# Kernel optimization log

Hardware: AMD Instinct MI355X
Metric: run time of the kernel (lower is better)

Reference implementation:

```python
import jax, jax.numpy as jnp
import numpy as np

E = 64        # first-level branches / experts
N_LEAF = 1024 # leaves per branch (item id = branch*N_LEAF + leaf; zero trajectory = (0,0))
K = 10        # output_list_size


def setup_inputs() -> dict:
    key = jax.random.key(0)
    ks = jax.random.split(key, 8)
    s = 0.05
    B, D, H = 256, 256, 512
    return {
        "state": jax.random.normal(ks[0], (B, D), jnp.float32),
        # root policy (outputs E branch logits)
        "rW1": jax.random.normal(ks[1], (D, H), jnp.float32) * s,
        "rb1": jnp.zeros((H,), jnp.float32),
        "rW2": jax.random.normal(ks[2], (H, H), jnp.float32) * s,
        "rb2": jnp.zeros((H,), jnp.float32),
        "rW3": jax.random.normal(ks[3], (H, E), jnp.float32) * s,
        "rb3": jnp.zeros((E,), jnp.float32),
        # stacked per-branch expert policies (each outputs N_LEAF logits)
        "eW1": jax.random.normal(ks[4], (E, D, H), jnp.float32) * s,
        "eb1": jnp.zeros((E, H), jnp.float32),
        "eW2": jax.random.normal(ks[5], (E, H, H), jnp.float32) * s,
        "eb2": jnp.zeros((E, H), jnp.float32),
        "eW3": jax.random.normal(ks[6], (E, H, N_LEAF), jnp.float32) * s,
        "eb3": jnp.zeros((E, N_LEAF), jnp.float32),
    }


def reference(state, rW1, rb1, rW2, rb2, rW3, rb3, eW1, eb1, eW2, eb2, eW3, eb3):
    # deterministic=True path, mask_items=None
    B = state.shape[0]
    relu = jax.nn.relu
    # root policy: MLP -> branch logits [B, E]
    h = relu(state @ rW1 + rb1)
    h = relu(h @ rW2 + rb2)
    root_logits = h @ rW3 + rb3
    idx = jnp.argmax(root_logits, axis=-1)                       # top-1 branch per sample [B]
    root_lp = jax.nn.log_softmax(root_logits, axis=-1)[jnp.arange(B), idx]  # [B]
    # top-1 routed expert forward: gather per-sample expert weights (MoE dispatch)
    h1 = relu(jnp.einsum('bi,bih->bh', state, eW1[idx]) + eb1[idx])
    h2 = relu(jnp.einsum('bh,bhg->bg', h1, eW2[idx]) + eb2[idx])
    logits = jnp.einsum('bg,bgn->bn', h2, eW3[idx]) + eb3[idx]   # [B, N_LEAF]
    lp = jax.nn.log_softmax(logits, axis=-1)
    # top-(k+1), then drop leaf 0 if this sample routed to branch 0 (the id-0 trajectory)
    _, top_idx = jax.lax.top_k(logits, K + 1)                    # [B, K+1]
    keep = ~((top_idx == 0) & (idx[:, None] == 0))
    order = jnp.argsort(~keep, axis=1, stable=True)              # kept entries first, order preserved
    item_idx = jnp.take_along_axis(top_idx, order[:, :K], axis=1)  # [B, K]
    final_lp = jnp.take_along_axis(lp, item_idx, axis=1) + root_lp[:, None]  # [B, K]
    traj = jnp.stack([jnp.broadcast_to(idx[:, None], (B, K)), item_idx], axis=-1)  # [B, K, 2]
    return traj, final_lp
```

## Files before the change

kernel.cpp:

```cpp
#include <hip/hip_runtime.h>
#include <math.h>

#define Bn 256
#define Dm 256
#define Hm 512
#define Em 64
#define NL 1024
#define TOPK 10
#define GS 8
#define MAXG 88

template<int IN, int OUT, int MT, int XPARTS, bool GROUPED>
__global__ __launch_bounds__(512) void dense_ks4(
        const float* __restrict__ X, const int* __restrict__ perm,
        const float* __restrict__ Bin, int bin_estride,
        const float* __restrict__ W, const int4* __restrict__ groups,
        float* __restrict__ Y) {
    constexpr int NW = 8, KQ = IN / 4, KCH = KQ / NW, CCH = 256, NR = 4;

    int e, p0, cnt;
    if (GROUPED) {
        const int4 g = groups[blockIdx.x];
        if (g.z == 0) return;
        e = g.x; p0 = g.y; cnt = g.z;
    } else {
        e = 0; p0 = blockIdx.x * MT; cnt = MT;
    }
    const int kq = blockIdx.z;
    const int kbase = kq * KQ;

    __shared__ float sxT[KQ * MT];
    __shared__ float part[NR * MT * CCH];
    const int tid = threadIdx.x;

    for (int j = tid; j < (KQ / 4) * MT; j += 512) {
        const int c  = j & (MT - 1);
        const int i4 = j / MT;
        float4 x = make_float4(0.f, 0.f, 0.f, 0.f);
        if (c < cnt) {
            const int row = perm ? perm[p0 + c] : (p0 + c);
            const size_t off = (size_t)row * IN + kbase + i4 * 4;
            x = *(const float4*)(X + off);
            #pragma unroll
            for (int pb = 1; pb < XPARTS; ++pb) {
                const float4 xp = *(const float4*)(X + (size_t)pb * Bn * IN + off);
                x.x += xp.x; x.y += xp.y; x.z += xp.z; x.w += xp.w;
            }
            if (Bin) {
                const float4 b = *(const float4*)(Bin + (size_t)e * bin_estride + kbase + i4 * 4);
                x.x = fmaxf(x.x + b.x, 0.f); x.y = fmaxf(x.y + b.y, 0.f);
                x.z = fmaxf(x.z + b.z, 0.f); x.w = fmaxf(x.w + b.w, 0.f);
            }
        }
        sxT[(i4 * 4 + 0) * MT + c] = x.x;
        sxT[(i4 * 4 + 1) * MT + c] = x.y;
        sxT[(i4 * 4 + 2) * MT + c] = x.z;
        sxT[(i4 * 4 + 3) * MT + c] = x.w;
    }
    __syncthreads();

    const int wave = tid >> 6, lane = tid & 63;
    const int colb = blockIdx.y * CCH;
    const int col  = colb + lane * 4;
    const int k0   = wave * KCH;
    const float* We = W + (size_t)e * IN * OUT + (size_t)(kbase + k0) * OUT + col;

    float acc[MT][4];
    #pragma unroll
    for (int c = 0; c < MT; ++c) { acc[c][0]=0.f; acc[c][1]=0.f; acc[c][2]=0.f; acc[c][3]=0.f; }

    #pragma unroll 4
    for (int i = 0; i < KCH; ++i) {
        const float4 w = *(const float4*)(We + (size_t)i * OUT);
        const float* xr = &sxT[(k0 + i) * MT];
        const float4 xa = *(const float4*)xr;
        const float4 xb = *(const float4*)(xr + 4);
        const float xs[8] = {xa.x, xa.y, xa.z, xa.w, xb.x, xb.y, xb.z, xb.w};
        #pragma unroll
        for (int c = 0; c < 8; ++c) {
            acc[c][0] = fmaf(xs[c], w.x, acc[c][0]);
            acc[c][1] = fmaf(xs[c], w.y, acc[c][1]);
            acc[c][2] = fmaf(xs[c], w.z, acc[c][2]);
            acc[c][3] = fmaf(xs[c], w.w, acc[c][3]);
        }
    }

    if (wave < NR) {
        #pragma unroll
        for (int c = 0; c < MT; ++c)
            *(float4*)&part[((wave * MT) + c) * CCH + lane * 4] = *(const float4*)acc[c];
    }
    __syncthreads();
    if (wave >= NR) {
        #pragma unroll
        for (int c = 0; c < MT; ++c) {
            float4* pp = (float4*)&part[(((wave - NR) * MT) + c) * CCH + lane * 4];
            float4 v = *pp;
            v.x += acc[c][0]; v.y += acc[c][1]; v.z += acc[c][2]; v.w += acc[c][3];
            *pp = v;
        }
    }
    __syncthreads();

    float* Yq = Y + (size_t)kq * Bn * OUT;
    for (int j = tid; j < MT * (CCH / 4); j += 512) {
        const int c = j / (CCH / 4);
        const int q = j % (CCH / 4);
        float4 s = *(const float4*)&part[c * CCH + q * 4];
        #pragma unroll
        for (int w = 1; w < NR; ++w) {
            const float4 p2 = *(const float4*)&part[((w * MT) + c) * CCH + q * 4];
            s.x += p2.x; s.y += p2.y; s.z += p2.z; s.w += p2.w;
        }
        if (c < cnt)
            *(float4*)(Yq + (size_t)(p0 + c) * OUT + colb + q * 4) = s;
    }
}

__global__ __launch_bounds__(512) void root3_ks(
        const float* __restrict__ H2, const float* __restrict__ Bin,
        const float* __restrict__ W, const float* __restrict__ bias,
        int* __restrict__ idx_out, float* __restrict__ rlp_out) {
    __shared__ float sxT[Hm * 8];
    __shared__ float part[8 * 8 * Em];
    __shared__ float fin[8][Em];
    const int tid = threadIdx.x;
    const int b0 = blockIdx.x * 8;

    for (int j = tid; j < (Hm / 4) * 8; j += 512) {
        const int c = j & 7, i4 = j >> 3;
        const size_t off = (size_t)(b0 + c) * Hm + i4 * 4;
        float4 x = *(const float4*)(H2 + off);
        #pragma unroll
        for (int pb = 1; pb < 4; ++pb) {
            const float4 xp = *(const float4*)(H2 + (size_t)pb * Bn * Hm + off);
            x.x += xp.x; x.y += xp.y; x.z += xp.z; x.w += xp.w;
        }
        const float4 b = *(const float4*)(Bin + i4 * 4);
        x.x = fmaxf(x.x + b.x, 0.f); x.y = fmaxf(x.y + b.y, 0.f);
        x.z = fmaxf(x.z + b.z, 0.f); x.w = fmaxf(x.w + b.w, 0.f);
        sxT[(i4 * 4 + 0) * 8 + c] = x.x;
        sxT[(i4 * 4 + 1) * 8 + c] = x.y;
        sxT[(i4 * 4 + 2) * 8 + c] = x.z;
        sxT[(i4 * 4 + 3) * 8 + c] = x.w;
    }
    __syncthreads();

    const int wave = tid >> 6, lane = tid & 63;
    const int k0 = wave * 64;
    float acc[8] = {0.f,0.f,0.f,0.f,0.f,0.f,0.f,0.f};
    #pragma unroll 4
    for (int i = 0; i < 64; ++i) {
        const float w = W[(size_t)(k0 + i) * Em + lane];
        const float* xr = &sxT[(k0 + i) * 8];
        const float4 xa = *(const float4*)xr;
        const float4 xb = *(const float4*)(xr + 4);
        acc[0] = fmaf(xa.x, w, acc[0]); acc[1] = fmaf(xa.y, w, acc[1]);
        acc[2] = fmaf(xa.z, w, acc[2]); acc[3] = fmaf(xa.w, w, acc[3]);
        acc[4] = fmaf(xb.x, w, acc[4]); acc[5] = fmaf(xb.y, w, acc[5]);
        acc[6] = fmaf(xb.z, w, acc[6]); acc[7] = fmaf(xb.w, w, acc[7]);
    }
    #pragma unroll
    for (int c = 0; c < 8; ++c) part[(wave * 8 + c) * Em + lane] = acc[c];
    __syncthreads();
    {
        const int c = wave, colj = lane;
        float s = bias[colj];
        #pragma unroll
        for (int w = 0; w < 8; ++w) s += part[(w * 8 + c) * Em + colj];
        fin[c][colj] = s;
    }
    __syncthreads();
    {
        const int c = wave;
        const float a0 = fin[c][lane];
        float v = a0; int bi = lane;
        #pragma unroll
        for (int off = 32; off; off >>= 1) {
            const float ov = __shfl_xor(v, off);
            const int   oi = __shfl_xor(bi, off);
            if (ov > v || (ov == v && oi < bi)) { v = ov; bi = oi; }
        }
        float ssum = expf(a0 - v);
        #pragma unroll
        for (int off = 32; off; off >>= 1) ssum += __shfl_xor(ssum, off);
        if (lane == 0) { idx_out[b0 + c] = bi; rlp_out[b0 + c] = -logf(ssum); }
    }
}

__global__ __launch_bounds__(256) void routing_kernel(const int* __restrict__ idx,
        int* __restrict__ perm, int4* __restrict__ groups) {
    __shared__ int cnt[Em];
    __shared__ int offs[Em];
    __shared__ int gtot;
    const int tid = threadIdx.x;
    if (tid < Em) cnt[tid] = 0;
    __syncthreads();
    const int e = idx[tid];
    const int r = atomicAdd(&cnt[e], 1);
    __syncthreads();
    if (tid < Em) {
        const int n  = cnt[tid];
        const int ng = (n + GS - 1) / GS;
        int s1 = n, s2 = ng;
        #pragma unroll
        for (int off = 1; off < 64; off <<= 1) {
            const int t1 = __shfl_up(s1, off);
            const int t2 = __shfl_up(s2, off);
            if (tid >= off) { s1 += t1; s2 += t2; }
        }
        offs[tid] = s1 - n;
        if (tid == Em - 1) gtot = s2;
        const int gb = s2 - ng;
        for (int k = 0; k < ng; ++k)
            groups[gb + k] = make_int4(tid, (s1 - n) + k * GS, min(GS, n - k * GS), 0);
    }
    __syncthreads();
    for (int g = gtot + tid; g < MAXG; g += 256) groups[g] = make_int4(0, 0, 0, 0);
    perm[offs[e] + r] = tid;
}

__global__ __launch_bounds__(512) void topk_kernel(
        const float* __restrict__ logitsQ, const float* __restrict__ eb3,
        const int* __restrict__ perm, const int* __restrict__ idx,
        const float* __restrict__ rlp, float* __restrict__ out) {
    __shared__ float sl[NL];
    __shared__ float redA[8];
    __shared__ float redB[8];
    __shared__ float bcast[2];
    const int p = blockIdx.x;
    const int tid = threadIdx.x;
    const int b = perm[p];
    const int e = idx[b];

    const size_t off = (size_t)p * NL + tid * 2;
    float2 v2 = *(const float2*)(logitsQ + off);
    #pragma unroll
    for (int pb = 1; pb < 4; ++pb) {
        const float2 vp = *(const float2*)(logitsQ + (size_t)pb * Bn * NL + off);
        v2.x += vp.x; v2.y += vp.y;
    }
    const float2 b2 = *(const float2*)(eb3 + (size_t)e * NL + tid * 2);
    v2.x += b2.x; v2.y += b2.y;
    sl[tid * 2] = v2.x; sl[tid * 2 + 1] = v2.y;

    float m = fmaxf(v2.x, v2.y);
    #pragma unroll
    for (int off2 = 32; off2; off2 >>= 1) m = fmaxf(m, __shfl_xor(m, off2));
    const int wave = tid >> 6;
    if ((tid & 63) == 0) redA[wave] = m;
    __syncthreads();
    if (tid == 0) {
        float mm = redA[0];
        #pragma unroll
        for (int w = 1; w < 8; ++w) mm = fmaxf(mm, redA[w]);
        bcast[0] = mm;
    }
    __syncthreads();
    m = bcast[0];

    float s = expf(v2.x - m) + expf(v2.y - m);
    #pragma unroll
    for (int off2 = 32; off2; off2 >>= 1) s += __shfl_xor(s, off2);
    if ((tid & 63) == 0) redB[wave] = s;
    __syncthreads();
    if (tid == 0) {
        float ss = 0.f;
        #pragma unroll
        for (int w = 0; w < 8; ++w) ss += redB[w];
        bcast[1] = m + logf(ss);
    }
    __syncthreads();
    const float logZ = bcast[1];

    if (tid < 64) {
        float vals[16];
        #pragma unroll
        for (int q = 0; q < 16; ++q) vals[q] = sl[tid * 16 + q];
        float selv[11];
        int   seli[11];
        for (int t = 0; t < 11; ++t) {
            float v = -INFINITY; int bq = 0;
            #pragma unroll
            for (int q = 0; q < 16; ++q) {
                if (vals[q] > v) { v = vals[q]; bq = q; }
            }
            int gi = tid * 16 + bq;
            #pragma unroll
            for (int off2 = 32; off2; off2 >>= 1) {
                const float ov = __shfl_xor(v, off2);
                const int   oi = __shfl_xor(gi, off2);
                if (ov > v || (ov == v && oi < gi)) { v = ov; gi = oi; }
            }
            selv[t] = v;
            seli[t] = gi;
            if ((gi >> 4) == tid) vals[gi & 15] = -INFINITY;
        }
        if (tid == 0) {
            const float rl = rlp[b];
            int c2 = 0;
            for (int t = 0; t < 11 && c2 < TOPK; ++t) {
                if (seli[t] == 0 && e == 0) continue;
                out[(b * TOPK + c2) * 2 + 0] = (float)e;
                out[(b * TOPK + c2) * 2 + 1] = (float)seli[t];
                out[Bn * TOPK * 2 + b * TOPK + c2] = selv[t] - logZ + rl;
                ++c2;
            }
        }
    }
}

extern "C" void kernel_launch(void* const* d_in, const int* in_sizes, int n_in,
                              void* d_out, int out_size, void* d_ws, size_t ws_size,
                              hipStream_t stream) {
    const float* state = (const float*)d_in[0];
    const float* rW1   = (const float*)d_in[1];
    const float* rb1   = (const float*)d_in[2];
    const float* rW2   = (const float*)d_in[3];
    const float* rb2   = (const float*)d_in[4];
    const float* rW3   = (const float*)d_in[5];
    const float* rb3   = (const float*)d_in[6];
    const float* eW1   = (const float*)d_in[7];
    const float* eb1   = (const float*)d_in[8];
    const float* eW2   = (const float*)d_in[9];
    const float* eb2   = (const float*)d_in[10];
    const float* eW3   = (const float*)d_in[11];
    const float* eb3   = (const float*)d_in[12];
    float* out = (float*)d_out;

    float* h1p    = (float*)d_ws;
    float* h2p    = h1p + 4 * Bn * Hm;
    float* eh1p   = h2p + 4 * Bn * Hm;
    float* eh2p   = eh1p + 4 * Bn * Hm;
    float* logp   = eh2p + 4 * Bn * Hm;
    float* rlp    = logp + 4 * Bn * NL;
    int*   idxp   = (int*)(rlp + Bn);
    int*   perm   = idxp + Bn;
    int4*  groups = (int4*)(perm + Bn);

    dense_ks4<Dm, Hm, 8, 1, false><<<dim3(Bn / 8, Hm / 256, 4), 512, 0, stream>>>(
        state, nullptr, nullptr, 0, rW1, nullptr, h1p);
    dense_ks4<Hm, Hm, 8, 4, false><<<dim3(Bn / 8, Hm / 256, 4), 512, 0, stream>>>(
        h1p, nullptr, rb1, 0, rW2, nullptr, h2p);
    root3_ks<<<Bn / 8, 512, 0, stream>>>(h2p, rb2, rW3, rb3, idxp, rlp);
    routing_kernel<<<1, 256, 0, stream>>>(idxp, perm, groups);
    dense_ks4<Dm, Hm, 8, 1, true><<<dim3(MAXG, Hm / 256, 4), 512, 0, stream>>>(
        state, perm, nullptr, 0, eW1, groups, eh1p);
    dense_ks4<Hm, Hm, 8, 4, true><<<dim3(MAXG, Hm / 256, 4), 512, 0, stream>>>(
        eh1p, nullptr, eb1, Hm, eW2, groups, eh2p);
    dense_ks4<Hm, NL, 8, 4, true><<<dim3(MAXG, NL / 256, 4), 512, 0, stream>>>(
        eh2p, nullptr, eb2, Hm, eW3, groups, logp);
    topk_kernel<<<Bn, 512, 0, stream>>>(logp, eb3, perm, idxp, rlp, out);
}
```

Baseline: 82.17 us.

## Fuse routing into root output kernel via last-block atomic counter

The separate single-block routing kernel is removed. Its work now runs inside the root third-layer kernel, in whichever block finishes last, detected with an atomic counter and threadfence. The counter is reset by the first dense kernel. The root kernel also goes from 8 to 4 rows per block, doubling the grid to 64 blocks, and the dense kernel's inner loop unroll is raised from 4 to 8. This saves one kernel launch and the gap between launches, at the cost of a fence and a serialized tail in the final block.

After: 89.19 us. 1.09x slower.

```diff
diff --git a/kernel.cpp b/kernel.cpp
--- a/kernel.cpp
+++ b/kernel.cpp
@@ -15,8 +15,11 @@
         const float* __restrict__ X, const int* __restrict__ perm,
         const float* __restrict__ Bin, int bin_estride,
         const float* __restrict__ W, const int4* __restrict__ groups,
-        float* __restrict__ Y) {
+        int* zctr, float* __restrict__ Y) {
     constexpr int NW = 8, KQ = IN / 4, KCH = KQ / NW, CCH = 256, NR = 4;
+
+    if (zctr && threadIdx.x == 0 && blockIdx.x == 0 && blockIdx.y == 0 && blockIdx.z == 0)
+        atomicExch(zctr, 0);
 
     int e, p0, cnt;
     if (GROUPED) {
@@ -69,7 +72,7 @@
     #pragma unroll
     for (int c = 0; c < MT; ++c) { acc[c][0]=0.f; acc[c][1]=0.f; acc[c][2]=0.f; acc[c][3]=0.f; }
 
-    #pragma unroll 4
+    #pragma unroll 8
     for (int i = 0; i < KCH; ++i) {
         const float4 w = *(const float4*)(We + (size_t)i * OUT);
         const float* xr = &sxT[(k0 + i) * MT];
@@ -117,18 +120,23 @@
     }
 }
 
-__global__ __launch_bounds__(512) void root3_ks(
+__global__ __launch_bounds__(512) void root3_route(
         const float* __restrict__ H2, const float* __restrict__ Bin,
         const float* __restrict__ W, const float* __restrict__ bias,
-        int* __restrict__ idx_out, float* __restrict__ rlp_out) {
-    __shared__ float sxT[Hm * 8];
-    __shared__ float part[8 * 8 * Em];
-    __shared__ float fin[8][Em];
+        int* __restrict__ idx_out, float* __restrict__ rlp_out,
+        int* __restrict__ perm, int4* __restrict__ groups, int* __restrict__ ctr) {
+    __shared__ float sxT[Hm * 4];
+    __shared__ float part[8 * 4 * Em];
+    __shared__ float fin[4][Em];
+    __shared__ int sflag;
+    __shared__ int cnt[Em];
+    __shared__ int offs[Em];
+    __shared__ int gtot;
     const int tid = threadIdx.x;
-    const int b0 = blockIdx.x * 8;
-
-    for (int j = tid; j < (Hm / 4) * 8; j += 512) {
-        const int c = j & 7, i4 = j >> 3;
+    const int b0 = blockIdx.x * 4;
+
+    {
+        const int c = tid & 3, i4 = tid >> 2;
         const size_t off = (size_t)(b0 + c) * Hm + i4 * 4;
         float4 x = *(const float4*)(H2 + off);
         #pragma unroll
@@ -139,39 +147,39 @@
         const float4 b = *(const float4*)(Bin + i4 * 4);
         x.x = fmaxf(x.x + b.x, 0.f); x.y = fmaxf(x.y + b.y, 0.f);
         x.z = fmaxf(x.z + b.z, 0.f); x.w = fmaxf(x.w + b.w, 0.f);
-        sxT[(i4 * 4 + 0) * 8 + c] = x.x;
-        sxT[(i4 * 4 + 1) * 8 + c] = x.y;
-        sxT[(i4 * 4 + 2) * 8 + c] = x.z;
-        sxT[(i4 * 4 + 3) * 8 + c] = x.w;
+        sxT[(i4 * 4 + 0) * 4 + c] = x.x;
+        sxT[(i4 * 4 + 1) * 4 + c] = x.y;
+        sxT[(i4 * 4 + 2) * 4 + c] = x.z;
+        sxT[(i4 * 4 + 3) * 4 + c] = x.w;
     }
     __syncthreads();
 
     const int wave = tid >> 6, lane = tid & 63;
-    const int k0 = wave * 64;
-    float acc[8] = {0.f,0.f,0.f,0.f,0.f,0.f,0.f,0.f};
-    #pragma unroll 4
-    for (int i = 0; i < 64; ++i) {
-        const float w = W[(size_t)(k0 + i) * Em + lane];
-        const float* xr = &sxT[(k0 + i) * 8];
-        const float4 xa = *(const float4*)xr;
-        const float4 xb = *(const float4*)(xr + 4);
-        acc[0] = fmaf(xa.x, w, acc[0]); acc[1] = fmaf(xa.y, w, acc[1]);
-        acc[2] = fmaf(xa.z, w, acc[2]); acc[3] = fmaf(xa.w, w, acc[3]);
-        acc[4] = fmaf(xb.x, w, acc[4]); acc[5] = fmaf(xb.y, w, acc[5]);
-        acc[6] = fmaf(xb.z, w, acc[6]); acc[7] = fmaf(xb.w, w, acc[7]);
-    }
-    #pragma unroll
-    for (int c = 0; c < 8; ++c) part[(wave * 8 + c) * Em + lane] = acc[c];
-    __syncthreads();
     {
-        const int c = wave, colj = lane;
+        const int k0 = wave * 64;
+        float acc[4] = {0.f, 0.f, 0.f, 0.f};
+        #pragma unroll 8
+        for (int i = 0; i < 64; ++i) {
+            const float w = W[(size_t)(k0 + i) * Em + lane];
+            const float4 xa = *(const float4*)&sxT[(k0 + i) * 4];
+            acc[0] = fmaf(xa.x, w, acc[0]); acc[1] = fmaf(xa.y, w, acc[1]);
+            acc[2] = fmaf(xa.z, w, acc[2]); acc[3] = fmaf(xa.w, w, acc[3]);
+        }
+        #pragma unroll
+        for (int c = 0; c < 4; ++c) part[(wave * 4 + c) * Em + lane] = acc[c];
+    }
+    __syncthreads();
+
+    if (tid < 256) {
+        const int c = tid >> 6, colj = tid & 63;
         float s = bias[colj];
         #pragma unroll
-        for (int w = 0; w < 8; ++w) s += part[(w * 8 + c) * Em + colj];
+        for (int w = 0; w < 8; ++w) s += part[(w * 4 + c) * Em + colj];
         fin[c][colj] = s;
     }
     __syncthreads();
-    {
+
+    if (tid < 256) {
         const int c = wave;
         const float a0 = fin[c][lane];
         float v = a0; int bi = lane;
@@ -186,38 +194,39 @@
         for (int off = 32; off; off >>= 1) ssum += __shfl_xor(ssum, off);
         if (lane == 0) { idx_out[b0 + c] = bi; rlp_out[b0 + c] = -logf(ssum); }
     }
-}
-
-__global__ __launch_bounds__(256) void routing_kernel(const int* __restrict__ idx,
-        int* __restrict__ perm, int4* __restrict__ groups) {
-    __shared__ int cnt[Em];
-    __shared__ int offs[Em];
-    __shared__ int gtot;
-    const int tid = threadIdx.x;
-    if (tid < Em) cnt[tid] = 0;
-    __syncthreads();
-    const int e = idx[tid];
-    const int r = atomicAdd(&cnt[e], 1);
-    __syncthreads();
-    if (tid < Em) {
-        const int n  = cnt[tid];
-        const int ng = (n + GS - 1) / GS;
-        int s1 = n, s2 = ng;
-        #pragma unroll
-        for (int off = 1; off < 64; off <<= 1) {
-            const int t1 = __shfl_up(s1, off);
-            const int t2 = __shfl_up(s2, off);
-            if (tid >= off) { s1 += t1; s2 += t2; }
-        }
-        offs[tid] = s1 - n;
-        if (tid == Em - 1) gtot = s2;
-        const int gb = s2 - ng;
-        for (int k = 0; k < ng; ++k)
-            groups[gb + k] = make_int4(tid, (s1 - n) + k * GS, min(GS, n - k * GS), 0);
-    }
-    __syncthreads();
-    for (int g = gtot + tid; g < MAXG; g += 256) groups[g] = make_int4(0, 0, 0, 0);
-    perm[offs[e] + r] = tid;
+
+    __syncthreads();
+    __threadfence();
+    __syncthreads();
+    if (tid == 0) sflag = (atomicAdd(ctr, 1) == (int)gridDim.x - 1);
+    __syncthreads();
+    if (sflag) {
+        __threadfence();
+        if (tid < Em) cnt[tid] = 0;
+        __syncthreads();
+        int e = -1, r = -1;
+        if (tid < Bn) { e = idx_out[tid]; r = atomicAdd(&cnt[e], 1); }
+        __syncthreads();
+        if (tid < Em) {
+            const int n  = cnt[tid];
+            const int ng = (n + GS - 1) / GS;
+            int s1 = n, s2 = ng;
+            #pragma unroll
+            for (int off = 1; off < 64; off <<= 1) {
+                const int t1 = __shfl_up(s1, off);
+                const int t2 = __shfl_up(s2, off);
+                if (tid >= off) { s1 += t1; s2 += t2; }
+            }
+            offs[tid] = s1 - n;
+            if (tid == Em - 1) gtot = s2;
+            const int gb = s2 - ng;
+            for (int k = 0; k < ng; ++k)
+                groups[gb + k] = make_int4(tid, (s1 - n) + k * GS, min(GS, n - k * GS), 0);
+        }
+        __syncthreads();
+        for (int g = gtot + tid; g < MAXG; g += 512) groups[g] = make_int4(0, 0, 0, 0);
+        if (tid < Bn) perm[offs[e] + r] = tid;
+    }
 }
 
 __global__ __launch_bounds__(512) void topk_kernel(
@@ -337,18 +346,19 @@
     int*   idxp   = (int*)(rlp + Bn);
     int*   perm   = idxp + Bn;
     int4*  groups = (int4*)(perm + Bn);
+    int*   ctr    = (int*)(groups + MAXG);
 
     dense_ks4<Dm, Hm, 8, 1, false><<<dim3(Bn / 8, Hm / 256, 4), 512, 0, stream>>>(
-        state, nullptr, nullptr, 0, rW1, nullptr, h1p);
+        state, nullptr, nullptr, 0, rW1, nullptr, ctr, h1p);
     dense_ks4<Hm, Hm, 8, 4, false><<<dim3(Bn / 8, Hm / 256, 4), 512, 0, stream>>>(
-        h1p, nullptr, rb1, 0, rW2, nullptr, h2p);
-    root3_ks<<<Bn / 8, 512, 0, stream>>>(h2p, rb2, rW3, rb3, idxp, rlp);
-    routing_kernel<<<1, 256, 0, stream>>>(idxp, perm, groups);
+        h1p, nullptr, rb1, 0, rW2, nullptr, nullptr, h2p);
+    root3_route<<<Bn / 4, 512, 0, stream>>>(h2p, rb2, rW3, rb3, idxp, rlp,
+                                            perm, groups, ctr);
     dense_ks4<Dm, Hm, 8, 1, true><<<dim3(MAXG, Hm / 256, 4), 512, 0, stream>>>(
-        state, perm, nullptr, 0, eW1, groups, eh1p);
+        state, perm, nullptr, 0, eW1, groups, nullptr, eh1p);
     dense_ks4<Hm, Hm, 8, 4, true><<<dim3(MAXG, Hm / 256, 4), 512, 0, stream>>>(
-        eh1p, nullptr, eb1, Hm, eW2, groups, eh2p);
+        eh1p, nullptr, eb1, Hm, eW2, groups, nullptr, eh2p);
     dense_ks4<Hm, NL, 8, 4, true><<<dim3(MAXG, NL / 256, 4), 512, 0, stream>>>(
-        eh2p, nullptr, eb2, Hm, eW3, groups, logp);
+        eh2p, nullptr, eb2, Hm, eW3, groups, nullptr, logp);
     topk_kernel<<<Bn, 512, 0, stream>>>(logp, eb3, perm, idxp, rlp, out);
 }
```

## Fuse root policy MLP into a single kernel with shared-memory activations

Applied to the files above, without the earlier changes.

Replaces the three root-policy kernels (two split-K dense layers plus the final logits/argmax kernel) with one fused kernel in which each block handles 4 samples and keeps the hidden activations in shared memory. This removes two kernel launches and the global round-trips of the split-K partial buffers. In exchange, each block streams the full rW1/rW2 weights with only 4-sample reuse across 64 blocks, so parallelism per layer is lower and weight traffic through L2 is higher than in the tiled split-K version.

After: 115.3 us. 40.4% more time.

```diff
diff --git a/kernel.cpp b/kernel.cpp
--- a/kernel.cpp
+++ b/kernel.cpp
@@ -9,6 +9,81 @@
 #define TOPK 10
 #define GS 8
 #define MAXG 88
+
+__global__ __launch_bounds__(512) void root_fused(
+        const float* __restrict__ state,
+        const float* __restrict__ rW1, const float* __restrict__ rb1,
+        const float* __restrict__ rW2, const float* __restrict__ rb2,
+        const float* __restrict__ rW3, const float* __restrict__ rb3,
+        int* __restrict__ idx_out, float* __restrict__ rlp_out) {
+    __shared__ float sx[4 * Dm];
+    __shared__ float h1[4][Hm];
+    __shared__ float h2[4][Hm];
+    const int tid = threadIdx.x;
+    const int b0 = blockIdx.x * 4;
+
+    if (tid < 256) {
+        const int c = tid >> 6, i4 = tid & 63;
+        const float4 x = *(const float4*)(state + (size_t)(b0 + c) * Dm + i4 * 4);
+        *(float4*)&sx[c * Dm + i4 * 4] = x;
+    }
+    __syncthreads();
+
+    {
+        float a0 = 0.f, a1 = 0.f, a2 = 0.f, a3 = 0.f;
+        #pragma unroll 8
+        for (int i = 0; i < Dm; ++i) {
+            const float w = rW1[(size_t)i * Hm + tid];
+            a0 = fmaf(sx[0 * Dm + i], w, a0);
+            a1 = fmaf(sx[1 * Dm + i], w, a1);
+            a2 = fmaf(sx[2 * Dm + i], w, a2);
+            a3 = fmaf(sx[3 * Dm + i], w, a3);
+        }
+        const float b = rb1[tid];
+        h1[0][tid] = fmaxf(a0 + b, 0.f);
+        h1[1][tid] = fmaxf(a1 + b, 0.f);
+        h1[2][tid] = fmaxf(a2 + b, 0.f);
+        h1[3][tid] = fmaxf(a3 + b, 0.f);
+    }
+    __syncthreads();
+
+    {
+        float a0 = 0.f, a1 = 0.f, a2 = 0.f, a3 = 0.f;
+        #pragma unroll 8
+        for (int i = 0; i < Hm; ++i) {
+            const float w = rW2[(size_t)i * Hm + tid];
+            a0 = fmaf(h1[0][i], w, a0);
+            a1 = fmaf(h1[1][i], w, a1);
+            a2 = fmaf(h1[2][i], w, a2);
+            a3 = fmaf(h1[3][i], w, a3);
+        }
+        const float b = rb2[tid];
+        h2[0][tid] = fmaxf(a0 + b, 0.f);
+        h2[1][tid] = fmaxf(a1 + b, 0.f);
+        h2[2][tid] = fmaxf(a2 + b, 0.f);
+        h2[3][tid] = fmaxf(a3 + b, 0.f);
+    }
+    __syncthreads();
+
+    if (tid < 256) {
+        const int c = tid >> 6, lane = tid & 63;
+        float acc = rb3[lane];
+        #pragma unroll 8
+        for (int i = 0; i < Hm; ++i)
+            acc = fmaf(h2[c][i], rW3[(size_t)i * Em + lane], acc);
+        float v = acc; int bi = lane;
+        #pragma unroll
+        for (int off = 32; off; off >>= 1) {
+            const float ov = __shfl_xor(v, off);
+            const int   oi = __shfl_xor(bi, off);
+            if (ov > v || (ov == v && oi < bi)) { v = ov; bi = oi; }
+        }
+        float ssum = expf(acc - v);
+        #pragma unroll
+        for (int off = 32; off; off >>= 1) ssum += __shfl_xor(ssum, off);
+        if (lane == 0) { idx_out[b0 + c] = bi; rlp_out[b0 + c] = -logf(ssum); }
+    }
+}
 
 template<int IN, int OUT, int MT, int XPARTS, bool GROUPED>
 __global__ __launch_bounds__(512) void dense_ks4(
@@ -114,77 +189,6 @@
         }
         if (c < cnt)
             *(float4*)(Yq + (size_t)(p0 + c) * OUT + colb + q * 4) = s;
-    }
-}
-
-__global__ __launch_bounds__(512) void root3_ks(
-        const float* __restrict__ H2, const float* __restrict__ Bin,
-        const float* __restrict__ W, const float* __restrict__ bias,
-        int* __restrict__ idx_out, float* __restrict__ rlp_out) {
-    __shared__ float sxT[Hm * 8];
-    __shared__ float part[8 * 8 * Em];
-    __shared__ float fin[8][Em];
-    const int tid = threadIdx.x;
-    const int b0 = blockIdx.x * 8;
-
-    for (int j = tid; j < (Hm / 4) * 8; j += 512) {
-        const int c = j & 7, i4 = j >> 3;
-        const size_t off = (size_t)(b0 + c) * Hm + i4 * 4;
-        float4 x = *(const float4*)(H2 + off);
-        #pragma unroll
-        for (int pb = 1; pb < 4; ++pb) {
-            const float4 xp = *(const float4*)(H2 + (size_t)pb * Bn * Hm + off);
-            x.x += xp.x; x.y += xp.y; x.z += xp.z; x.w += xp.w;
-        }
-        const float4 b = *(const float4*)(Bin + i4 * 4);
-        x.x = fmaxf(x.x + b.x, 0.f); x.y = fmaxf(x.y + b.y, 0.f);
-        x.z = fmaxf(x.z + b.z, 0.f); x.w = fmaxf(x.w + b.w, 0.f);
-        sxT[(i4 * 4 + 0) * 8 + c] = x.x;
-        sxT[(i4 * 4 + 1) * 8 + c] = x.y;
-        sxT[(i4 * 4 + 2) * 8 + c] = x.z;
-        sxT[(i4 * 4 + 3) * 8 + c] = x.w;
-    }
-    __syncthreads();
-
-    const int wave = tid >> 6, lane = tid & 63;
-    const int k0 = wave * 64;
-    float acc[8] = {0.f,0.f,0.f,0.f,0.f,0.f,0.f,0.f};
-    #pragma unroll 4
-    for (int i = 0; i < 64; ++i) {
-        const float w = W[(size_t)(k0 + i) * Em + lane];
-        const float* xr = &sxT[(k0 + i) * 8];
-        const float4 xa = *(const float4*)xr;
-        const float4 xb = *(const float4*)(xr + 4);
-        acc[0] = fmaf(xa.x, w, acc[0]); acc[1] = fmaf(xa.y, w, acc[1]);
-        acc[2] = fmaf(xa.z, w, acc[2]); acc[3] = fmaf(xa.w, w, acc[3]);
-        acc[4] = fmaf(xb.x, w, acc[4]); acc[5] = fmaf(xb.y, w, acc[5]);
-        acc[6] = fmaf(xb.z, w, acc[6]); acc[7] = fmaf(xb.w, w, acc[7]);
-    }
-    #pragma unroll
-    for (int c = 0; c < 8; ++c) part[(wave * 8 + c) * Em + lane] = acc[c];
-    __syncthreads();
-    {
-        const int c = wave, colj = lane;
-        float s = bias[colj];
-        #pragma unroll
-        for (int w = 0; w < 8; ++w) s += part[(w * 8 + c) * Em + colj];
-        fin[c][colj] = s;
-    }
-    __syncthreads();
-    {
-        const int c = wave;
-        const float a0 = fin[c][lane];
-        float v = a0; int bi = lane;
-        #pragma unroll
-        for (int off = 32; off; off >>= 1) {
-            const float ov = __shfl_xor(v, off);
-            const int   oi = __shfl_xor(bi, off);
-            if (ov > v || (ov == v && oi < bi)) { v = ov; bi = oi; }
-        }
-        float ssum = expf(a0 - v);
-        #pragma unroll
-        for (int off = 32; off; off >>= 1) ssum += __shfl_xor(ssum, off);
-        if (lane == 0) { idx_out[b0 + c] = bi; rlp_out[b0 + c] = -logf(ssum); }
     }
 }
 
@@ -328,9 +332,7 @@
     const float* eb3   = (const float*)d_in[12];
     float* out = (float*)d_out;
 
-    float* h1p    = (float*)d_ws;
-    float* h2p    = h1p + 4 * Bn * Hm;
-    float* eh1p   = h2p + 4 * Bn * Hm;
+    float* eh1p   = (float*)d_ws;
     float* eh2p   = eh1p + 4 * Bn * Hm;
     float* logp   = eh2p + 4 * Bn * Hm;
     float* rlp    = logp + 4 * Bn * NL;
@@ -338,11 +340,8 @@
     int*   perm   = idxp + Bn;
     int4*  groups = (int4*)(perm + Bn);
 
-    dense_ks4<Dm, Hm, 8, 1, false><<<dim3(Bn / 8, Hm / 256, 4), 512, 0, stream>>>(
-        state, nullptr, nullptr, 0, rW1, nullptr, h1p);
-    dense_ks4<Hm, Hm, 8, 4, false><<<dim3(Bn / 8, Hm / 256, 4), 512, 0, stream>>>(
-        h1p, nullptr, rb1, 0, rW2, nullptr, h2p);
-    root3_ks<<<Bn / 8, 512, 0, stream>>>(h2p, rb2, rW3, rb3, idxp, rlp);
+    root_fused<<<Bn / 4, 512, 0, stream>>>(state, rW1, rb1, rW2, rb2, rW3, rb3,
+                                           idxp, rlp);
     routing_kernel<<<1, 256, 0, stream>>>(idxp, perm, groups);
     dense_ks4<Dm, Hm, 8, 1, true><<<dim3(MAXG, Hm / 256, 4), 512, 0, stream>>>(
         state, perm, nullptr, 0, eW1, groups, eh1p);
```
